# Performance work log

Measured on AMD Instinct MI355X. Metric: run time of the kernel, lower is better.

Reference implementation:

```python
import jax, jax.numpy as jnp
import numpy as np

N = 50000          # nodes
E = 800000         # edges (avg degree 16)
D_IN = 128
D_HID = 128
D_OUT = 64
NUM_GRAPHS = 64


def setup_inputs() -> dict:
    key = jax.random.key(0)
    ks = jax.random.split(key, 10)
    x = jax.random.normal(ks[0], (N, D_IN), dtype=jnp.float32)
    edge_index = jax.random.randint(ks[1], (2, E), 0, N, dtype=jnp.int64)
    batch = jnp.sort(jax.random.randint(ks[2], (N,), 0, NUM_GRAPHS, dtype=jnp.int64))
    def glorot(k, fan_in, fan_out):
        s = np.float32(np.sqrt(6.0 / (fan_in + fan_out)))
        return jax.random.uniform(k, (fan_in, fan_out), jnp.float32, -s, s)
    return {
        "x": x,
        "edge_index": edge_index,
        "batch": batch,
        "W1": glorot(ks[3], D_IN, D_HID),  "b1": jnp.zeros((D_HID,), jnp.float32),
        "W2": glorot(ks[4], D_HID, D_HID), "b2": jnp.zeros((D_HID,), jnp.float32),
        "W3": glorot(ks[5], D_HID, D_OUT), "b3": jnp.zeros((D_OUT,), jnp.float32),
    }


def _gcn_conv(x, W, b, src, dst, dis):
    # GCNConv: D^{-1/2}(A+I)D^{-1/2} X W + b  (self-loops handled analytically)
    h = x @ W                                   # [N, out]
    norm = dis[src] * dis[dst]                  # [E]
    agg = jax.ops.segment_sum(h[src] * norm[:, None], dst, num_segments=N)
    return agg + h * (dis * dis)[:, None] + b   # self-loop term + bias


def reference(x, edge_index, batch, W1, b1, W2, b2, W3, b3):
    src, dst = edge_index[0], edge_index[1]
    # degree with self-loop (matches PyG add_self_loops + gcn_norm)
    deg = jnp.zeros((N,), jnp.float32).at[dst].add(1.0) + 1.0
    dis = jax.lax.rsqrt(deg)                    # deg >= 1, no inf handling needed

    h = jax.nn.relu(_gcn_conv(x, W1, b1, src, dst, dis))
    h = jax.nn.relu(_gcn_conv(h, W2, b2, src, dst, dis))
    features = _gcn_conv(h, W3, b3, src, dst, dis)   # [N, D_OUT]

    sums = jax.ops.segment_sum(features, batch, num_segments=NUM_GRAPHS)
    cnts = jax.ops.segment_sum(jnp.ones((N,), jnp.float32), batch, num_segments=NUM_GRAPHS)
    avg_pool = sums / jnp.maximum(cnts, 1.0)[:, None]  # [NUM_GRAPHS, D_OUT]
    return features, avg_pool
```

## Files before the change

kernel.cpp:

```cpp
#include <hip/hip_runtime.h>


constexpr int KDIM = 128;
constexpr int NGRAPH = 64;

__device__ __forceinline__ unsigned bf16rne(float f) {
  unsigned u = __float_as_uint(f);
  return (u + 0x7fffu + ((u >> 16) & 1u)) >> 16;
}
__device__ __forceinline__ unsigned packbf2(float a, float b) {
  return bf16rne(a) | (bf16rne(b) << 16);
}

__global__ void k_init(int* __restrict__ counts, int n) {
  int i = blockIdx.x * blockDim.x + threadIdx.x;
  int stride = gridDim.x * blockDim.x;
  for (int j = i; j < n; j += stride) counts[j] = 0;
}

__global__ void k_hist(const int* __restrict__ src, const int* __restrict__ dst,
                       int* __restrict__ counts, int e, int n) {
  int i = blockIdx.x * blockDim.x + threadIdx.x;
  int stride = gridDim.x * blockDim.x;
  for (int j = i; j < e; j += stride) {
    int s = src[j], d = dst[j];
    if ((unsigned)s < (unsigned)n && (unsigned)d < (unsigned)n)
      atomicAdd(&counts[d], 1);
  }
}

__global__ void k_dis(const int* __restrict__ counts, float* __restrict__ dis, int n) {
  int i = blockIdx.x * blockDim.x + threadIdx.x;
  int stride = gridDim.x * blockDim.x;
  for (int j = i; j < n; j += stride)
    dis[j] = rsqrtf((float)counts[j] + 1.0f);
}

__global__ void k_scan_block(const int* __restrict__ in, int* __restrict__ outExcl,
                             int* __restrict__ blockSums, int n) {
  __shared__ int s[256];
  int tid = threadIdx.x;
  int i = blockIdx.x * 256 + tid;
  int v = (i < n) ? in[i] : 0;
  int x = v;
  s[tid] = x;
  __syncthreads();
  for (int off = 1; off < 256; off <<= 1) {
    int t = (tid >= off) ? s[tid - off] : 0;
    __syncthreads();
    x += t;
    s[tid] = x;
    __syncthreads();
  }
  if (i < n) outExcl[i] = x - v;
  if (tid == 255) blockSums[blockIdx.x] = x;
}

__global__ void k_scan_offsets(int* __restrict__ bs, int nb) {
  __shared__ int s[256];
  int tid = threadIdx.x;
  int v = (tid < nb) ? bs[tid] : 0;
  int x = v;
  s[tid] = x;
  __syncthreads();
  for (int off = 1; off < 256; off <<= 1) {
    int t = (tid >= off) ? s[tid - off] : 0;
    __syncthreads();
    x += t;
    s[tid] = x;
    __syncthreads();
  }
  if (tid < nb) bs[tid] = x - v;
  if (tid == nb - 1) bs[256] = x;
}

__global__ void k_scan_add(int* __restrict__ row_start, const int* __restrict__ bs,
                           int* __restrict__ cursor, int n) {
  int i = blockIdx.x * blockDim.x + threadIdx.x;
  int stride = gridDim.x * blockDim.x;
  for (int j = i; j < n; j += stride) {
    int r = row_start[j] + bs[j >> 8];
    row_start[j] = r;
    cursor[j] = r;
  }
  if (i == 0) row_start[n] = bs[256];
}

__global__ void k_scatter(const int* __restrict__ src, const int* __restrict__ dst,
                          int* __restrict__ cursor, int* __restrict__ colA,
                          int e, int n) {
  int i = blockIdx.x * blockDim.x + threadIdx.x;
  int stride = gridDim.x * blockDim.x;
  for (int j = i; j < e; j += stride) {
    int s = src[j], d = dst[j];
    if ((unsigned)s < (unsigned)n && (unsigned)d < (unsigned)n) {
      int pos = atomicAdd(&cursor[d], 1);
      colA[pos] = s;
    }
  }
}

template <int DOUT>
__global__ __launch_bounds__(256) void k_gemm2b(const float* __restrict__ X,
                                                const float* __restrict__ W,
                                                unsigned short* __restrict__ Hb,
                                                int n) {
  __shared__ float xT[32][128];
  __shared__ float Wl[32][64];
  const int tid = threadIdx.x;
  const int tr = tid & 15;
  const int tc = tid >> 4;
  const int rowBase = blockIdx.x * 128;
  const int colBase = blockIdx.y * 64;

  float acc[8][4];
#pragma unroll
  for (int i = 0; i < 8; ++i)
#pragma unroll
    for (int j = 0; j < 4; ++j) acc[i][j] = 0.f;

  const int sr = tid >> 1;
  const int kh = (tid & 1) * 16;
  const int srow = min(rowBase + sr, n - 1);
  const float* xsrc = X + (size_t)srow * KDIM + kh;

  for (int k0 = 0; k0 < KDIM / 32; ++k0) {
    {
      const float4* s4 = reinterpret_cast<const float4*>(xsrc + k0 * 32);
      float4 v0 = s4[0], v1 = s4[1], v2 = s4[2], v3 = s4[3];
      xT[kh + 0][sr] = v0.x;  xT[kh + 1][sr] = v0.y;
      xT[kh + 2][sr] = v0.z;  xT[kh + 3][sr] = v0.w;
      xT[kh + 4][sr] = v1.x;  xT[kh + 5][sr] = v1.y;
      xT[kh + 6][sr] = v1.z;  xT[kh + 7][sr] = v1.w;
      xT[kh + 8][sr] = v2.x;  xT[kh + 9][sr] = v2.y;
      xT[kh + 10][sr] = v2.z; xT[kh + 11][sr] = v2.w;
      xT[kh + 12][sr] = v3.x; xT[kh + 13][sr] = v3.y;
      xT[kh + 14][sr] = v3.z; xT[kh + 15][sr] = v3.w;
    }
#pragma unroll
    for (int q = 0; q < 2; ++q) {
      int f4 = tid + q * 256;
      int k = f4 >> 4;
      int c4 = f4 & 15;
      *reinterpret_cast<float4*>(&Wl[k][c4 * 4]) = *reinterpret_cast<const float4*>(
          W + (size_t)(k0 * 32 + k) * DOUT + colBase + c4 * 4);
    }
    __syncthreads();
#pragma unroll 8
    for (int k = 0; k < 32; ++k) {
      float4 xa = *reinterpret_cast<const float4*>(&xT[k][tr * 4]);
      float4 xb = *reinterpret_cast<const float4*>(&xT[k][64 + tr * 4]);
      float4 wv = *reinterpret_cast<const float4*>(&Wl[k][tc * 4]);
      const float xs[8] = {xa.x, xa.y, xa.z, xa.w, xb.x, xb.y, xb.z, xb.w};
      const float ws[4] = {wv.x, wv.y, wv.z, wv.w};
#pragma unroll
      for (int i = 0; i < 8; ++i)
#pragma unroll
        for (int j = 0; j < 4; ++j) acc[i][j] = fmaf(xs[i], ws[j], acc[i][j]);
    }
    __syncthreads();
  }

#pragma unroll
  for (int i = 0; i < 8; ++i) {
    int row = rowBase + ((i < 4) ? (tr * 4 + i) : (64 + tr * 4 + i - 4));
    if (row < n) {
      uint2 o;
      o.x = packbf2(acc[i][0], acc[i][1]);
      o.y = packbf2(acc[i][2], acc[i][3]);
      *reinterpret_cast<uint2*>(Hb + (size_t)row * DOUT + colBase + tc * 4) = o;
    }
  }
}

template <int D, bool RELU>
__global__ __launch_bounds__(256) void k_agg6(const unsigned short* __restrict__ Hb,
                                              const int* __restrict__ row_start,
                                              const int* __restrict__ colA,
                                              const float* __restrict__ dis,
                                              const float* __restrict__ bias,
                                              float* __restrict__ OUT, int n) {
  const int wave = threadIdx.x >> 6;
  const int lane = threadIdx.x & 63;
  const int slot = wave >> 1;
  const int half = wave & 1;
  const int node = blockIdx.x * 2 + slot;
  constexpr int C = D / 64;
  __shared__ float red[4][D];

  if (node < n) {
    const int beg = row_start[node];
    const int end = row_start[node + 1];
    const float di = dis[node];
    float acc[C];
#pragma unroll
    for (int c = 0; c < C; ++c) acc[c] = 0.f;

    int e = beg + half;
    for (; e + 2 < end; e += 4) {
      const int s0 = colA[e], s1 = colA[e + 2];
      const float n0 = dis[s0] * di, n1 = dis[s1] * di;
      if constexpr (C == 2) {
        const unsigned u0 =
            reinterpret_cast<const unsigned*>(Hb + (size_t)s0 * D)[lane];
        const unsigned u1 =
            reinterpret_cast<const unsigned*>(Hb + (size_t)s1 * D)[lane];
        acc[0] = fmaf(__uint_as_float(u0 << 16), n0, acc[0]);
        acc[1] = fmaf(__uint_as_float(u0 & 0xffff0000u), n0, acc[1]);
        acc[0] = fmaf(__uint_as_float(u1 << 16), n1, acc[0]);
        acc[1] = fmaf(__uint_as_float(u1 & 0xffff0000u), n1, acc[1]);
      } else {
        const unsigned v0 = Hb[(size_t)s0 * D + lane];
        const unsigned v1 = Hb[(size_t)s1 * D + lane];
        acc[0] = fmaf(__uint_as_float(v0 << 16), n0, acc[0]);
        acc[0] = fmaf(__uint_as_float(v1 << 16), n1, acc[0]);
      }
    }
    for (; e < end; e += 2) {
      const int s0 = colA[e];
      const float n0 = dis[s0] * di;
      if constexpr (C == 2) {
        const unsigned u0 =
            reinterpret_cast<const unsigned*>(Hb + (size_t)s0 * D)[lane];
        acc[0] = fmaf(__uint_as_float(u0 << 16), n0, acc[0]);
        acc[1] = fmaf(__uint_as_float(u0 & 0xffff0000u), n0, acc[1]);
      } else {
        const unsigned v0 = Hb[(size_t)s0 * D + lane];
        acc[0] = fmaf(__uint_as_float(v0 << 16), n0, acc[0]);
      }
    }
#pragma unroll
    for (int c = 0; c < C; ++c) red[wave][C * lane + c] = acc[c];
  } else {
#pragma unroll
    for (int c = 0; c < C; ++c) red[wave][C * lane + c] = 0.f;
  }
  __syncthreads();
  if (half == 0 && node < n) {
    const float di = dis[node];
    const float di2 = di * di;
    float hs[C];
    if constexpr (C == 2) {
      const unsigned u =
          reinterpret_cast<const unsigned*>(Hb + (size_t)node * D)[lane];
      hs[0] = __uint_as_float(u << 16);
      hs[1] = __uint_as_float(u & 0xffff0000u);
    } else {
      hs[0] = __uint_as_float((unsigned)Hb[(size_t)node * D + lane] << 16);
    }
    float* o = OUT + (size_t)node * D + C * lane;
    const float* bi = bias + C * lane;
#pragma unroll
    for (int c = 0; c < C; ++c) {
      float v = red[wave][C * lane + c] + red[wave + 1][C * lane + c] +
                hs[c] * di2 + bi[c];
      if (RELU) v = fmaxf(v, 0.f);
      o[c] = v;
    }
  }
}

__global__ __launch_bounds__(256) void k_pool2(const float* __restrict__ F,
                                               const int* __restrict__ batch,
                                               float* __restrict__ out, int n) {
  const int g = blockIdx.x;
  __shared__ int sb[2];
  if (threadIdx.x < 2) {
    int target = g + threadIdx.x;
    int lo = 0, hi = n;
    while (lo < hi) {
      int mid = (lo + hi) >> 1;
      if (batch[mid] < target) lo = mid + 1; else hi = mid;
    }
    sb[threadIdx.x] = lo;
  }
  __syncthreads();
  const int beg = sb[0], end = sb[1];
  const int wave = threadIdx.x >> 6;
  const int lane = threadIdx.x & 63;
  float acc = 0.f;
  for (int node = beg + wave; node < end; node += 4)
    acc += F[(size_t)node * 64 + lane];
  __shared__ float red[4][64];
  red[wave][lane] = acc;
  __syncthreads();
  if (wave == 0) {
    float v = (red[0][lane] + red[1][lane]) + (red[2][lane] + red[3][lane]);
    out[g * 64 + lane] = v / fmaxf((float)(end - beg), 1.f);
  }
}

extern "C" void kernel_launch(void* const* d_in, const int* in_sizes, int n_in,
                              void* d_out, int out_size, void* d_ws, size_t ws_size,
                              hipStream_t stream) {
  const float* x     = (const float*)d_in[0];
  const int*   ei    = (const int*)d_in[1];
  const int*   batch = (const int*)d_in[2];
  const float* W1 = (const float*)d_in[3];
  const float* b1 = (const float*)d_in[4];
  const float* W2 = (const float*)d_in[5];
  const float* b2 = (const float*)d_in[6];
  const float* W3 = (const float*)d_in[7];
  const float* b3 = (const float*)d_in[8];

  const int n = in_sizes[0] / KDIM;
  const int e = in_sizes[1] / 2;
  const int* src = ei;
  const int* dst = ei + e;

  char* p = (char*)d_ws;
  size_t off = 0;
  auto carve = [&](size_t bytes) {
    char* r = p + off;
    off = (off + bytes + 255) & ~(size_t)255;
    return r;
  };
  unsigned short* Hb = (unsigned short*)carve((size_t)n * KDIM * 2);
  float* F           = (float*)carve((size_t)n * KDIM * 4);
  float* dis         = (float*)carve((size_t)n * 4);
  int*   counts      = (int*)carve((size_t)n * 4);
  int*   row_start   = (int*)carve((size_t)(n + 1) * 4);
  int*   cursor      = (int*)carve((size_t)n * 4);
  int*   colA        = (int*)carve((size_t)e * 4);
  int*   blockSums   = (int*)carve(512 * 4);
  (void)ws_size;

  const int nb1 = (n + 255) / 256;
  const int GS = 1024;

  k_init<<<GS, 256, 0, stream>>>(counts, n);
  k_hist<<<GS, 256, 0, stream>>>(src, dst, counts, e, n);
  k_dis<<<nb1, 256, 0, stream>>>(counts, dis, n);
  k_scan_block<<<nb1, 256, 0, stream>>>(counts, row_start, blockSums, n);
  k_scan_offsets<<<1, 256, 0, stream>>>(blockSums, nb1);
  k_scan_add<<<nb1, 256, 0, stream>>>(row_start, blockSums, cursor, n);
  k_scatter<<<GS, 256, 0, stream>>>(src, dst, cursor, colA, e, n);

  const int rowBlocks = (n + 127) / 128;
  const int aggGrid = (n + 1) / 2;

  k_gemm2b<128><<<dim3(rowBlocks, 2), 256, 0, stream>>>(x, W1, Hb, n);
  k_agg6<128, true><<<aggGrid, 256, 0, stream>>>(Hb, row_start, colA, dis, b1, F, n);
  k_gemm2b<128><<<dim3(rowBlocks, 2), 256, 0, stream>>>(F, W2, Hb, n);
  k_agg6<128, true><<<aggGrid, 256, 0, stream>>>(Hb, row_start, colA, dis, b2, F, n);
  k_gemm2b<64><<<dim3(rowBlocks, 1), 256, 0, stream>>>(F, W3, Hb, n);
  k_agg6<64, false><<<aggGrid, 256, 0, stream>>>(Hb, row_start, colA, dis, b3,
                                                 (float*)d_out, n);
  k_pool2<<<NGRAPH, 256, 0, stream>>>((const float*)d_out, batch,
                                      (float*)d_out + (size_t)n * 64, n);
}
```

Baseline: 514.9 us.

## Aggregate two nodes per wave without shared-memory reduction

Restructures the CSR aggregation kernel so each wave handles two destination nodes at once, interleaving their neighbor gathers with two accumulators per node. Previously two waves split each node's edges and combined partial sums through shared memory behind a block barrier. Removing the LDS reduction and __syncthreads and keeping four gathers in flight per iteration is meant to raise memory-level parallelism, at the cost of load imbalance when the two nodes' degrees differ.

```diff
diff --git a/kernel.cpp b/kernel.cpp
--- a/kernel.cpp
+++ b/kernel.cpp
@@ -10,6 +10,12 @@
 }
 __device__ __forceinline__ unsigned packbf2(float a, float b) {
   return bf16rne(a) | (bf16rne(b) << 16);
+}
+__device__ __forceinline__ float bflo(unsigned u) {
+  return __uint_as_float(u << 16);
+}
+__device__ __forceinline__ float bfhi(unsigned u) {
+  return __uint_as_float(u & 0xffff0000u);
 }
 
 __global__ void k_init(int* __restrict__ counts, int n) {
@@ -174,88 +180,95 @@
 }
 
 template <int D, bool RELU>
-__global__ __launch_bounds__(256) void k_agg6(const unsigned short* __restrict__ Hb,
-                                              const int* __restrict__ row_start,
-                                              const int* __restrict__ colA,
-                                              const float* __restrict__ dis,
-                                              const float* __restrict__ bias,
-                                              float* __restrict__ OUT, int n) {
+__global__ __launch_bounds__(256, 4) void k_agg7(
+    const unsigned short* __restrict__ Hb, const int* __restrict__ row_start,
+    const int* __restrict__ colA, const float* __restrict__ dis,
+    const float* __restrict__ bias, float* __restrict__ OUT, int n) {
+  constexpr int C = D / 64;
   const int wave = threadIdx.x >> 6;
   const int lane = threadIdx.x & 63;
-  const int slot = wave >> 1;
-  const int half = wave & 1;
-  const int node = blockIdx.x * 2 + slot;
-  constexpr int C = D / 64;
-  __shared__ float red[4][D];
-
-  if (node < n) {
-    const int beg = row_start[node];
-    const int end = row_start[node + 1];
-    const float di = dis[node];
-    float acc[C];
-#pragma unroll
-    for (int c = 0; c < C; ++c) acc[c] = 0.f;
-
-    int e = beg + half;
-    for (; e + 2 < end; e += 4) {
-      const int s0 = colA[e], s1 = colA[e + 2];
-      const float n0 = dis[s0] * di, n1 = dis[s1] * di;
-      if constexpr (C == 2) {
-        const unsigned u0 =
-            reinterpret_cast<const unsigned*>(Hb + (size_t)s0 * D)[lane];
-        const unsigned u1 =
-            reinterpret_cast<const unsigned*>(Hb + (size_t)s1 * D)[lane];
-        acc[0] = fmaf(__uint_as_float(u0 << 16), n0, acc[0]);
-        acc[1] = fmaf(__uint_as_float(u0 & 0xffff0000u), n0, acc[1]);
-        acc[0] = fmaf(__uint_as_float(u1 << 16), n1, acc[0]);
-        acc[1] = fmaf(__uint_as_float(u1 & 0xffff0000u), n1, acc[1]);
-      } else {
-        const unsigned v0 = Hb[(size_t)s0 * D + lane];
-        const unsigned v1 = Hb[(size_t)s1 * D + lane];
-        acc[0] = fmaf(__uint_as_float(v0 << 16), n0, acc[0]);
-        acc[0] = fmaf(__uint_as_float(v1 << 16), n1, acc[0]);
-      }
-    }
-    for (; e < end; e += 2) {
-      const int s0 = colA[e];
-      const float n0 = dis[s0] * di;
-      if constexpr (C == 2) {
-        const unsigned u0 =
-            reinterpret_cast<const unsigned*>(Hb + (size_t)s0 * D)[lane];
-        acc[0] = fmaf(__uint_as_float(u0 << 16), n0, acc[0]);
-        acc[1] = fmaf(__uint_as_float(u0 & 0xffff0000u), n0, acc[1]);
-      } else {
-        const unsigned v0 = Hb[(size_t)s0 * D + lane];
-        acc[0] = fmaf(__uint_as_float(v0 << 16), n0, acc[0]);
-      }
-    }
-#pragma unroll
-    for (int c = 0; c < C; ++c) red[wave][C * lane + c] = acc[c];
-  } else {
-#pragma unroll
-    for (int c = 0; c < C; ++c) red[wave][C * lane + c] = 0.f;
-  }
-  __syncthreads();
-  if (half == 0 && node < n) {
-    const float di = dis[node];
-    const float di2 = di * di;
-    float hs[C];
-    if constexpr (C == 2) {
-      const unsigned u =
-          reinterpret_cast<const unsigned*>(Hb + (size_t)node * D)[lane];
-      hs[0] = __uint_as_float(u << 16);
-      hs[1] = __uint_as_float(u & 0xffff0000u);
-    } else {
-      hs[0] = __uint_as_float((unsigned)Hb[(size_t)node * D + lane] << 16);
-    }
-    float* o = OUT + (size_t)node * D + C * lane;
-    const float* bi = bias + C * lane;
+  const int nA = blockIdx.x * 8 + wave * 2;
+  const int nB = nA + 1;
+  const bool vA = nA < n, vB = nB < n;
+
+  int eA = vA ? row_start[nA] : 0, endA = vA ? row_start[nA + 1] : 0;
+  int eB = vB ? row_start[nB] : 0, endB = vB ? row_start[nB + 1] : 0;
+  const float diA = vA ? dis[nA] : 0.f;
+  const float diB = vB ? dis[nB] : 0.f;
+
+  float aA0[C], aA1[C], aB0[C], aB1[C];
+#pragma unroll
+  for (int c = 0; c < C; ++c) { aA0[c] = 0.f; aA1[c] = 0.f; aB0[c] = 0.f; aB1[c] = 0.f; }
+
+  auto hload = [&](int s) -> unsigned {
+    if constexpr (C == 2)
+      return reinterpret_cast<const unsigned*>(Hb + (size_t)s * D)[lane];
+    else
+      return (unsigned)Hb[(size_t)s * D + lane];
+  };
+  auto fma1 = [&](float* acc, unsigned u, float w) {
+    acc[0] = fmaf(bflo(u), w, acc[0]);
+    if constexpr (C == 2) acc[1] = fmaf(bfhi(u), w, acc[1]);
+  };
+
+  while (eA + 1 < endA && eB + 1 < endB) {
+    const int sA0 = colA[eA], sA1 = colA[eA + 1];
+    const int sB0 = colA[eB], sB1 = colA[eB + 1];
+    const float wA0 = dis[sA0] * diA, wA1 = dis[sA1] * diA;
+    const float wB0 = dis[sB0] * diB, wB1 = dis[sB1] * diB;
+    const unsigned hA0 = hload(sA0), hA1 = hload(sA1);
+    const unsigned hB0 = hload(sB0), hB1 = hload(sB1);
+    fma1(aA0, hA0, wA0);
+    fma1(aA1, hA1, wA1);
+    fma1(aB0, hB0, wB0);
+    fma1(aB1, hB1, wB1);
+    eA += 2; eB += 2;
+  }
+  while (eA + 1 < endA) {
+    const int s0 = colA[eA], s1 = colA[eA + 1];
+    const float w0 = dis[s0] * diA, w1 = dis[s1] * diA;
+    const unsigned h0 = hload(s0), h1 = hload(s1);
+    fma1(aA0, h0, w0);
+    fma1(aA1, h1, w1);
+    eA += 2;
+  }
+  if (eA < endA) {
+    const int s0 = colA[eA];
+    fma1(aA0, hload(s0), dis[s0] * diA);
+  }
+  while (eB + 1 < endB) {
+    const int s0 = colA[eB], s1 = colA[eB + 1];
+    const float w0 = dis[s0] * diB, w1 = dis[s1] * diB;
+    const unsigned h0 = hload(s0), h1 = hload(s1);
+    fma1(aB0, h0, w0);
+    fma1(aB1, h1, w1);
+    eB += 2;
+  }
+  if (eB < endB) {
+    const int s0 = colA[eB];
+    fma1(aB0, hload(s0), dis[s0] * diB);
+  }
+
+  if (vA) {
+    const unsigned u = hload(nA);
+    const float di2 = diA * diA;
 #pragma unroll
     for (int c = 0; c < C; ++c) {
-      float v = red[wave][C * lane + c] + red[wave + 1][C * lane + c] +
-                hs[c] * di2 + bi[c];
+      float h = (c == 0) ? bflo(u) : bfhi(u);
+      float v = aA0[c] + aA1[c] + h * di2 + bias[C * lane + c];
       if (RELU) v = fmaxf(v, 0.f);
-      o[c] = v;
+      OUT[(size_t)nA * D + C * lane + c] = v;
+    }
+  }
+  if (vB) {
+    const unsigned u = hload(nB);
+    const float di2 = diB * diB;
+#pragma unroll
+    for (int c = 0; c < C; ++c) {
+      float h = (c == 0) ? bflo(u) : bfhi(u);
+      float v = aB0[c] + aB1[c] + h * di2 + bias[C * lane + c];
+      if (RELU) v = fmaxf(v, 0.f);
+      OUT[(size_t)nB * D + C * lane + c] = v;
     }
   }
 }
@@ -337,14 +350,14 @@
   k_scatter<<<GS, 256, 0, stream>>>(src, dst, cursor, colA, e, n);
 
   const int rowBlocks = (n + 127) / 128;
-  const int aggGrid = (n + 1) / 2;
+  const int aggGrid = (n + 7) / 8;
 
   k_gemm2b<128><<<dim3(rowBlocks, 2), 256, 0, stream>>>(x, W1, Hb, n);
-  k_agg6<128, true><<<aggGrid, 256, 0, stream>>>(Hb, row_start, colA, dis, b1, F, n);
+  k_agg7<128, true><<<aggGrid, 256, 0, stream>>>(Hb, row_start, colA, dis, b1, F, n);
   k_gemm2b<128><<<dim3(rowBlocks, 2), 256, 0, stream>>>(F, W2, Hb, n);
-  k_agg6<128, true><<<aggGrid, 256, 0, stream>>>(Hb, row_start, colA, dis, b2, F, n);
+  k_agg7<128, true><<<aggGrid, 256, 0, stream>>>(Hb, row_start, colA, dis, b2, F, n);
   k_gemm2b<64><<<dim3(rowBlocks, 1), 256, 0, stream>>>(F, W3, Hb, n);
-  k_agg6<64, false><<<aggGrid, 256, 0, stream>>>(Hb, row_start, colA, dis, b3,
+  k_agg7<64, false><<<aggGrid, 256, 0, stream>>>(Hb, row_start, colA, dis, b3,
                                                  (float*)d_out, n);
   k_pool2<<<NGRAPH, 256, 0, stream>>>((const float*)d_out, batch,
                                       (float*)d_out + (size_t)n * 64, n);
```

Measured after the change: 446.3 us. 1.15x faster.
